# Kernel tuning notes

Hardware: AMD Instinct MI355X
Metric: run time of the kernel (lower is better)

## Reference

```python
import jax, jax.numpy as jnp
import numpy as np


def setup_inputs() -> dict:
    key = jax.random.key(0)
    k1, k2, k3 = jax.random.split(key, 3)
    B, T, S, D = 16, 1024, 1024, 1024
    inp = jax.random.normal(k1, (B, T, D), dtype=jnp.float32)
    ctx = jax.random.normal(k2, (B, S, D), dtype=jnp.float32)
    # nn.Linear(dim, dim, bias=False) weight, applied as x @ W.T
    W_in = jax.random.normal(k3, (D, D), dtype=jnp.float32) * (1.0 / np.sqrt(D))
    return {"input": inp, "context": ctx, "W_in": W_in}


def reference(input, context, W_in):
    # h_t = linear_in(input): [B,T,D] @ W_in.T
    h_t = jnp.einsum("btd,ed->bte", input, W_in)
    # align scores: [B,T,S]
    align = jnp.einsum("btd,bsd->bts", h_t, context)
    align_vectors = jax.nn.softmax(align, axis=-1)
    # context-weighted sum: [B,T,D]
    attn_h = jnp.einsum("bts,bsd->btd", align_vectors, context)
    # non-one-step path: transpose(0,1)
    attn_h = jnp.transpose(attn_h, (1, 0, 2))          # [T,B,D]
    align_vectors = jnp.transpose(align_vectors, (1, 0, 2))  # [T,B,S]
    return attn_h, align_vectors
```

## Files before the change

kernel.cpp:

```cpp
#include <hip/hip_runtime.h>
#include <hip/hip_bf16.h>

using short8 = __attribute__((ext_vector_type(8))) short;
using half8  = __attribute__((ext_vector_type(8))) _Float16;
using f32x4  = __attribute__((ext_vector_type(4))) float;

constexpr int Bdim = 16;
constexpr int Tdim = 1024;
constexpr int Sdim = 1024;
constexpr int Ddim = 1024;

__device__ __forceinline__ unsigned short f2hu(float x) {
  _Float16 h = (_Float16)x;
  return __builtin_bit_cast(unsigned short, h);
}
__device__ __forceinline__ float hu2f(unsigned short u) {
  return (float)__builtin_bit_cast(_Float16, u);
}

__global__ void __launch_bounds__(256)
conv_kernel(const float* __restrict__ src, unsigned short* __restrict__ dst, int n4) {
  int i = blockIdx.x * blockDim.x + threadIdx.x;
  int stride = gridDim.x * blockDim.x;
  for (; i < n4; i += stride) {
    float4 v = reinterpret_cast<const float4*>(src)[i];
    ushort4 h;
    h.x = f2hu(v.x); h.y = f2hu(v.y); h.z = f2hu(v.z); h.w = f2hu(v.w);
    reinterpret_cast<ushort4*>(dst)[i] = h;
  }
}

__global__ void __launch_bounds__(256)
ctxprep_kernel(const float* __restrict__ ctx, unsigned short* __restrict__ ctx16,
               unsigned short* __restrict__ ctxT) {
  __shared__ float tile[64][65];
  int b = blockIdx.z;
  int d0 = blockIdx.x * 64, s0 = blockIdx.y * 64;
  const float* src = ctx + (size_t)b * Sdim * Ddim;
  unsigned short* dstS = ctx16 + (size_t)b * Sdim * Ddim;
  unsigned short* dstT = ctxT + (size_t)b * Ddim * Sdim;
  int tx = threadIdx.x & 15, ty = threadIdx.x >> 4;
  #pragma unroll
  for (int r = 0; r < 4; ++r) {
    int s = ty + r * 16;
    float4 v = reinterpret_cast<const float4*>(src + (size_t)(s0 + s) * Ddim + d0)[tx];
    ushort4 hs;
    hs.x = f2hu(v.x); hs.y = f2hu(v.y); hs.z = f2hu(v.z); hs.w = f2hu(v.w);
    reinterpret_cast<ushort4*>(dstS + (size_t)(s0 + s) * Ddim + d0)[tx] = hs;
    tile[s][tx * 4 + 0] = v.x; tile[s][tx * 4 + 1] = v.y;
    tile[s][tx * 4 + 2] = v.z; tile[s][tx * 4 + 3] = v.w;
  }
  __syncthreads();
  #pragma unroll
  for (int r = 0; r < 4; ++r) {
    int d = ty + r * 16;
    ushort4 o;
    o.x = f2hu(tile[tx * 4 + 0][d]);
    o.y = f2hu(tile[tx * 4 + 1][d]);
    o.z = f2hu(tile[tx * 4 + 2][d]);
    o.w = f2hu(tile[tx * 4 + 3][d]);
    reinterpret_cast<ushort4*>(dstT + (size_t)(d0 + d) * Sdim + s0)[tx] = o;
  }
}

__device__ __forceinline__ short8 fragr(const unsigned short* t, int row, int g0) {
  int pg = g0 ^ ((row >> 1) & 3);
  return *reinterpret_cast<const short8*>(t + row * 32 + pg * 8);
}

#define MFMAH(d, x, y)                                                          \
  d = __builtin_amdgcn_mfma_f32_16x16x32_f16(__builtin_bit_cast(half8, (x)),    \
                                             __builtin_bit_cast(half8, (y)), (d), 0, 0, 0)

#define GLOADLDS(g, l)                                                          \
  __builtin_amdgcn_global_load_lds((const __attribute__((address_space(1))) void*)(g), \
                                   (__attribute__((address_space(3))) void*)(l), 16, 0, 0)

template <int MODE>
__global__ void __launch_bounds__(512, 2)
gemmP(const unsigned short* __restrict__ Ag, const unsigned short* __restrict__ Bg,
      size_t aBatch, size_t bBatch, int mnShift,
      unsigned short* __restrict__ outHi, unsigned short* __restrict__ outLo,
      float* __restrict__ outF) {
  constexpr int NT = 16;
  __shared__ __align__(16) unsigned short lds[2 * 2 * 16384];

  const int hw = blockIdx.x;
  const int L  = (hw & 7) * 32 + (hw >> 3);
  const int bb = L >> mnShift;
  const int r  = L & ((1 << mnShift) - 1);
  const int m0 = (r >> 2) * 256;
  const int n0 = (r & 3) * 256;

  const int tid  = threadIdx.x;
  const int lane = tid & 63;
  const int w    = tid >> 6;
  const int wr   = (w >> 2) * 128;
  const int wc   = (w & 3) * 64;
  const int l15  = lane & 15;
  const int g0   = lane >> 4;
  const int r7   = l15 & 7;

  const int srow8 = tid >> 3;
  const int sg    = tid & 7;
  const int rs    = srow8 & 7;
  const unsigned short* spA = Ag + (size_t)bb * aBatch + (size_t)(m0 + srow8) * 1024 + ((sg ^ rs) * 8);
  const unsigned short* spB = Bg + (size_t)bb * bBatch + (size_t)(n0 + srow8) * 1024 + ((sg ^ rs) * 8);

  auto stage = [&](int buf, int kt) {
    #pragma unroll
    for (int i = 0; i < 4; ++i) {
      unsigned short* lb = lds + buf * 32768 + (srow8 + i * 64) * 64 + sg * 8;
      GLOADLDS(spA + (size_t)i * (64 * 1024) + kt * 64, lb);
      GLOADLDS(spB + (size_t)i * (64 * 1024) + kt * 64, lb + 16384);
    }
  };

  f32x4 acc[8][4];
  const f32x4 vzero = {0.f, 0.f, 0.f, 0.f};
  #pragma unroll
  for (int f = 0; f < 8; ++f)
    #pragma unroll
    for (int j = 0; j < 4; ++j) acc[f][j] = vzero;

  stage(0, 0);

  #pragma unroll 1
  for (int t = 0; t < NT; ++t) {
    stage((t + 1) & 1, (t + 1 < NT) ? (t + 1) : (NT - 1));
    asm volatile("s_waitcnt vmcnt(8)" ::: "memory");
    __builtin_amdgcn_s_barrier();
    asm volatile("" ::: "memory");
    const unsigned short* tb = lds + (t & 1) * 32768;
    const unsigned short* tB = tb + 16384;

    short8 bf[4][2];
    #pragma unroll
    for (int j = 0; j < 4; ++j)
      #pragma unroll
      for (int kk = 0; kk < 2; ++kk) {
        const int row = wc + j * 16 + l15;
        bf[j][kk] = *reinterpret_cast<const short8*>(tB + row * 64 + ((kk * 4 + g0) ^ r7) * 8);
      }
    #pragma unroll
    for (int fp = 0; fp < 4; ++fp) {
      short8 af[2][2];
      #pragma unroll
      for (int f2 = 0; f2 < 2; ++f2) {
        const int row = wr + (fp * 2 + f2) * 16 + l15;
        #pragma unroll
        for (int kk = 0; kk < 2; ++kk)
          af[f2][kk] = *reinterpret_cast<const short8*>(tb + row * 64 + ((kk * 4 + g0) ^ r7) * 8);
      }
      __builtin_amdgcn_s_setprio(1);
      #pragma unroll
      for (int f2 = 0; f2 < 2; ++f2)
        #pragma unroll
        for (int j = 0; j < 4; ++j)
          #pragma unroll
          for (int kk = 0; kk < 2; ++kk)
            MFMAH(acc[fp * 2 + f2][j], af[f2][kk], bf[j][kk]);
      __builtin_amdgcn_s_setprio(0);
    }
    asm volatile("s_waitcnt lgkmcnt(0)" ::: "memory");
    __builtin_amdgcn_sched_barrier(0);
    __builtin_amdgcn_s_barrier();
  }

  const int lr = (lane >> 4) * 4;
  const int lc = lane & 15;
  #pragma unroll
  for (int f = 0; f < 8; ++f)
    #pragma unroll
    for (int j = 0; j < 4; ++j)
      #pragma unroll
      for (int q = 0; q < 4; ++q) {
        int rr = m0 + wr + f * 16 + lr + q;
        int cc = n0 + wc + j * 16 + lc;
        float v = acc[f][j][q];
        if constexpr (MODE == 0) {
          unsigned short h = f2hu(v);
          unsigned short l = f2hu(v - hu2f(h));
          outHi[(size_t)rr * 1024 + cc] = h;
          outLo[(size_t)rr * 1024 + cc] = l;
        } else {
          outF[((size_t)rr * 16 + bb) * 1024 + cc] = v;
        }
      }
}

__global__ void __launch_bounds__(512, 2)
gemmU(const unsigned short* __restrict__ Ah, const unsigned short* __restrict__ Al,
      const unsigned short* __restrict__ Bh,
      size_t aBatch, size_t bBatch, int mnShift,
      float* __restrict__ outF) {
  constexpr int OPS = 3;
  constexpr int BUFSTRIDE = OPS * 8192;
  constexpr int NT = 32;
  __shared__ __align__(16) unsigned short lds[3 * BUFSTRIDE];

  const int hw = blockIdx.x;
  const int L  = (hw & 7) * 32 + (hw >> 3);
  const int bb = L >> mnShift;
  const int r  = L & ((1 << mnShift) - 1);
  const int m0 = (r >> 2) * 256;
  const int n0 = (r & 3) * 256;

  const int tid  = threadIdx.x;
  const int lane = tid & 63;
  const int w    = tid >> 6;
  const int wr   = (w >> 2) * 128;
  const int wc   = (w & 3) * 64;
  const int l15  = lane & 15;
  const int g0   = lane >> 4;

  const int srow = tid >> 2;
  const int scol = ((tid & 3) ^ ((srow >> 1) & 3)) * 8;
  const unsigned short* sp[3];
  {
    const size_t aOff = (size_t)bb * aBatch + (size_t)(m0 + srow) * 1024 + scol;
    const size_t bOff = (size_t)bb * bBatch + (size_t)(n0 + srow) * 1024 + scol;
    sp[0] = Ah + aOff; sp[1] = Al + aOff; sp[2] = Bh + bOff;
  }

  auto stage_tile = [&](int buf, int kt) {
    #pragma unroll
    for (int op = 0; op < OPS; ++op)
      #pragma unroll
      for (int h = 0; h < 2; ++h) {
        const unsigned short* g = sp[op] + (size_t)h * (128 * 1024) + kt * 32;
        unsigned short* l = lds + buf * BUFSTRIDE + op * 8192 + h * 4096 + tid * 8;
        GLOADLDS(g, l);
      }
  };

  f32x4 acc[8][4];
  const f32x4 vzero = {0.f, 0.f, 0.f, 0.f};
  #pragma unroll
  for (int f = 0; f < 8; ++f)
    #pragma unroll
    for (int j = 0; j < 4; ++j) acc[f][j] = vzero;

  short8 ah[4], al[4], b0[2], b1[2];

  stage_tile(0, 0);
  stage_tile(1, 1);

  #pragma unroll 1
  for (int t = 0; t < NT; ++t) {
    const unsigned short* tb = lds + (t % 3) * BUFSTRIDE;
    const unsigned short* tA = tb;
    const unsigned short* tAl = tb + 8192;
    const unsigned short* tB = tb + 16384;

    stage_tile((t + 2) % 3, (t + 2 < NT) ? (t + 2) : (NT - 1));
    asm volatile("s_waitcnt vmcnt(12)" ::: "memory");
    __builtin_amdgcn_s_barrier();
    asm volatile("" ::: "memory");

    #pragma unroll
    for (int f = 0; f < 4; ++f) {
      ah[f] = fragr(tA, wr + f * 16 + l15, g0);
      al[f] = fragr(tAl, wr + f * 16 + l15, g0);
    }
    #pragma unroll
    for (int j = 0; j < 2; ++j) b0[j] = fragr(tB, wc + j * 16 + l15, g0);
    __builtin_amdgcn_s_setprio(1);
    #pragma unroll
    for (int f = 0; f < 4; ++f)
      #pragma unroll
      for (int j = 0; j < 2; ++j) { MFMAH(acc[f][j], ah[f], b0[j]); MFMAH(acc[f][j], al[f], b0[j]); }
    __builtin_amdgcn_s_setprio(0);

    #pragma unroll
    for (int j = 0; j < 2; ++j) b1[j] = fragr(tB, wc + (j + 2) * 16 + l15, g0);
    __builtin_amdgcn_s_setprio(1);
    #pragma unroll
    for (int f = 0; f < 4; ++f)
      #pragma unroll
      for (int j = 0; j < 2; ++j) { MFMAH(acc[f][j + 2], ah[f], b1[j]); MFMAH(acc[f][j + 2], al[f], b1[j]); }
    __builtin_amdgcn_s_setprio(0);

    #pragma unroll
    for (int f = 0; f < 4; ++f) {
      ah[f] = fragr(tA, wr + 64 + f * 16 + l15, g0);
      al[f] = fragr(tAl, wr + 64 + f * 16 + l15, g0);
    }
    __builtin_amdgcn_s_setprio(1);
    #pragma unroll
    for (int f = 0; f < 4; ++f)
      #pragma unroll
      for (int j = 0; j < 2; ++j) { MFMAH(acc[4 + f][j], ah[f], b0[j]); MFMAH(acc[4 + f][j], al[f], b0[j]); }
    __builtin_amdgcn_s_setprio(0);

    __builtin_amdgcn_s_setprio(1);
    #pragma unroll
    for (int f = 0; f < 4; ++f)
      #pragma unroll
      for (int j = 0; j < 2; ++j) { MFMAH(acc[4 + f][j + 2], ah[f], b1[j]); MFMAH(acc[4 + f][j + 2], al[f], b1[j]); }
    __builtin_amdgcn_s_setprio(0);
    asm volatile("" ::: "memory");
    __builtin_amdgcn_s_barrier();
  }

  const int lr = (lane >> 4) * 4;
  const int lc = lane & 15;
  #pragma unroll
  for (int f = 0; f < 8; ++f)
    #pragma unroll
    for (int j = 0; j < 4; ++j)
      #pragma unroll
      for (int q = 0; q < 4; ++q) {
        int rr = m0 + wr + f * 16 + lr + q;
        int cc = n0 + wc + j * 16 + lc;
        outF[((size_t)rr * 16 + bb) * 1024 + cc] = acc[f][j][q];
      }
}

__global__ void __launch_bounds__(256)
softmax_kernel(float* __restrict__ av, unsigned short* __restrict__ p) {
  int row = blockIdx.x;
  int t = row >> 4, b = row & 15;
  float* a = av + (size_t)row * 1024;
  int tid = threadIdx.x, lane = tid & 63, wid = tid >> 6;
  float4 v = reinterpret_cast<float4*>(a)[tid];
  float mx = fmaxf(fmaxf(v.x, v.y), fmaxf(v.z, v.w));
  #pragma unroll
  for (int o = 1; o < 64; o <<= 1) mx = fmaxf(mx, __shfl_xor(mx, o));
  __shared__ float redM[4], redS[4];
  if (lane == 0) redM[wid] = mx;
  __syncthreads();
  mx = fmaxf(fmaxf(redM[0], redM[1]), fmaxf(redM[2], redM[3]));
  float e0 = __expf(v.x - mx), e1 = __expf(v.y - mx);
  float e2 = __expf(v.z - mx), e3 = __expf(v.w - mx);
  float s = (e0 + e1) + (e2 + e3);
  #pragma unroll
  for (int o = 1; o < 64; o <<= 1) s += __shfl_xor(s, o);
  if (lane == 0) redS[wid] = s;
  __syncthreads();
  s = (redS[0] + redS[1]) + (redS[2] + redS[3]);
  float inv = 1.0f / s;
  float4 o4;
  o4.x = e0 * inv; o4.y = e1 * inv; o4.z = e2 * inv; o4.w = e3 * inv;
  reinterpret_cast<float4*>(a)[tid] = o4;
  ushort4 pb;
  pb.x = f2hu(o4.x); pb.y = f2hu(o4.y); pb.z = f2hu(o4.z); pb.w = f2hu(o4.w);
  reinterpret_cast<ushort4*>(p + ((size_t)b * Tdim + t) * Sdim)[tid] = pb;
}

extern "C" void kernel_launch(void* const* d_in, const int* in_sizes, int n_in,
                              void* d_out, int out_size, void* d_ws, size_t ws_size,
                              hipStream_t stream) {
  const float* input = (const float*)d_in[0];
  const float* ctx   = (const float*)d_in[1];
  const float* Wt    = (const float*)d_in[2];
  float* attn_out  = (float*)d_out;
  float* align_out = attn_out + (size_t)Tdim * Bdim * Ddim;

  const size_t NE = (size_t)Bdim * Tdim * Ddim;
  unsigned short* x16 = (unsigned short*)d_ws;
  unsigned short* Wh  = x16 + NE;
  unsigned short* hh  = Wh + (size_t)Ddim * Ddim;
  unsigned short* hl  = hh + NE;
  unsigned short* ctxT = hl + NE;
  unsigned short* ctx16 = x16;
  unsigned short* p     = hh;

  conv_kernel<<<2048, 256, 0, stream>>>(input, x16, (int)(NE / 4));
  conv_kernel<<<512, 256, 0, stream>>>(Wt, Wh, (int)((size_t)Ddim * Ddim / 4));
  gemmP<0><<<256, 512, 0, stream>>>(x16, Wh, 0, 0, 8, hh, hl, nullptr);
  ctxprep_kernel<<<dim3(16, 16, Bdim), 256, 0, stream>>>(ctx, ctx16, ctxT);
  gemmU<<<256, 512, 0, stream>>>(hh, hl, ctx16, (size_t)Tdim * Ddim,
                                 (size_t)Sdim * Ddim, 4, align_out);
  softmax_kernel<<<Bdim * Tdim, 256, 0, stream>>>(align_out, p);
  gemmP<1><<<256, 512, 0, stream>>>(p, ctxT, (size_t)Tdim * Sdim,
                                    (size_t)Ddim * Sdim, 4, nullptr, nullptr, attn_out);
}
```

Baseline: 220.5 us.

## Restructure align GEMM with K=64 tiles, double-buffered A and single-buffered B

Replaces the triple-buffered K=32 align-score GEMM with a K=64 version. The hi/lo A tiles are double-buffered, while the B (context) tile sits in a single buffer that is refilled mid-iteration once every wave holds its B fragments in registers. This halves the number of main-loop iterations and barriers and uses a wider XOR swizzle for the 64-wide rows. In exchange it adds an extra barrier per iteration, keeps more fragments live in registers, and exposes the B load latency inside the loop.

```diff
diff --git a/kernel.cpp b/kernel.cpp
--- a/kernel.cpp
+++ b/kernel.cpp
@@ -61,11 +61,6 @@
     o.w = f2hu(tile[tx * 4 + 3][d]);
     reinterpret_cast<ushort4*>(dstT + (size_t)(d0 + d) * Sdim + s0)[tx] = o;
   }
-}
-
-__device__ __forceinline__ short8 fragr(const unsigned short* t, int row, int g0) {
-  int pg = g0 ^ ((row >> 1) & 3);
-  return *reinterpret_cast<const short8*>(t + row * 32 + pg * 8);
 }
 
 #define MFMAH(d, x, y)                                                          \
@@ -190,14 +185,12 @@
 }
 
 __global__ void __launch_bounds__(512, 2)
-gemmU(const unsigned short* __restrict__ Ah, const unsigned short* __restrict__ Al,
+gemmS(const unsigned short* __restrict__ Ah, const unsigned short* __restrict__ Al,
       const unsigned short* __restrict__ Bh,
       size_t aBatch, size_t bBatch, int mnShift,
       float* __restrict__ outF) {
-  constexpr int OPS = 3;
-  constexpr int BUFSTRIDE = OPS * 8192;
-  constexpr int NT = 32;
-  __shared__ __align__(16) unsigned short lds[3 * BUFSTRIDE];
+  constexpr int NT = 16;
+  __shared__ __align__(16) unsigned short lds[5 * 16384];
 
   const int hw = blockIdx.x;
   const int L  = (hw & 7) * 32 + (hw >> 3);
@@ -213,25 +206,30 @@
   const int wc   = (w & 3) * 64;
   const int l15  = lane & 15;
   const int g0   = lane >> 4;
-
-  const int srow = tid >> 2;
-  const int scol = ((tid & 3) ^ ((srow >> 1) & 3)) * 8;
-  const unsigned short* sp[3];
-  {
-    const size_t aOff = (size_t)bb * aBatch + (size_t)(m0 + srow) * 1024 + scol;
-    const size_t bOff = (size_t)bb * bBatch + (size_t)(n0 + srow) * 1024 + scol;
-    sp[0] = Ah + aOff; sp[1] = Al + aOff; sp[2] = Bh + bOff;
-  }
-
-  auto stage_tile = [&](int buf, int kt) {
-    #pragma unroll
-    for (int op = 0; op < OPS; ++op)
-      #pragma unroll
-      for (int h = 0; h < 2; ++h) {
-        const unsigned short* g = sp[op] + (size_t)h * (128 * 1024) + kt * 32;
-        unsigned short* l = lds + buf * BUFSTRIDE + op * 8192 + h * 4096 + tid * 8;
-        GLOADLDS(g, l);
-      }
+  const int r7   = l15 & 7;
+
+  const int srow8 = tid >> 3;
+  const int sg    = tid & 7;
+  const int rs    = srow8 & 7;
+  const size_t aRow = (size_t)bb * aBatch + (size_t)(m0 + srow8) * 1024 + ((sg ^ rs) * 8);
+  const unsigned short* spAh = Ah + aRow;
+  const unsigned short* spAl = Al + aRow;
+  const unsigned short* spB  = Bh + (size_t)bb * bBatch + (size_t)(n0 + srow8) * 1024 + ((sg ^ rs) * 8);
+
+  auto stageA = [&](int buf, int kt) {
+    #pragma unroll
+    for (int i = 0; i < 4; ++i) {
+      unsigned short* lb = lds + buf * 32768 + (srow8 + i * 64) * 64 + sg * 8;
+      GLOADLDS(spAh + (size_t)i * (64 * 1024) + kt * 64, lb);
+      GLOADLDS(spAl + (size_t)i * (64 * 1024) + kt * 64, lb + 16384);
+    }
+  };
+  auto stageB = [&](int kt) {
+    #pragma unroll
+    for (int i = 0; i < 4; ++i) {
+      unsigned short* lb = lds + 65536 + (srow8 + i * 64) * 64 + sg * 8;
+      GLOADLDS(spB + (size_t)i * (64 * 1024) + kt * 64, lb);
+    }
   };
 
   f32x4 acc[8][4];
@@ -241,65 +239,82 @@
     #pragma unroll
     for (int j = 0; j < 4; ++j) acc[f][j] = vzero;
 
-  short8 ah[4], al[4], b0[2], b1[2];
-
-  stage_tile(0, 0);
-  stage_tile(1, 1);
+  stageA(0, 0);
+  stageB(0);
 
   #pragma unroll 1
   for (int t = 0; t < NT; ++t) {
-    const unsigned short* tb = lds + (t % 3) * BUFSTRIDE;
-    const unsigned short* tA = tb;
-    const unsigned short* tAl = tb + 8192;
-    const unsigned short* tB = tb + 16384;
-
-    stage_tile((t + 2) % 3, (t + 2 < NT) ? (t + 2) : (NT - 1));
-    asm volatile("s_waitcnt vmcnt(12)" ::: "memory");
+    const int tn = (t + 1 < NT) ? t + 1 : NT - 1;
+    stageA((t + 1) & 1, tn);
+    asm volatile("s_waitcnt vmcnt(8)" ::: "memory");
     __builtin_amdgcn_s_barrier();
     asm volatile("" ::: "memory");
-
-    #pragma unroll
-    for (int f = 0; f < 4; ++f) {
-      ah[f] = fragr(tA, wr + f * 16 + l15, g0);
-      al[f] = fragr(tAl, wr + f * 16 + l15, g0);
-    }
-    #pragma unroll
-    for (int j = 0; j < 2; ++j) b0[j] = fragr(tB, wc + j * 16 + l15, g0);
+    const unsigned short* tA  = lds + (t & 1) * 32768;
+    const unsigned short* tAl = tA + 16384;
+    const unsigned short* tB  = lds + 65536;
+
+    short8 bf[4][2];
+    #pragma unroll
+    for (int j = 0; j < 4; ++j)
+      #pragma unroll
+      for (int kk = 0; kk < 2; ++kk) {
+        const int row = wc + j * 16 + l15;
+        bf[j][kk] = *reinterpret_cast<const short8*>(tB + row * 64 + ((kk * 4 + g0) ^ r7) * 8);
+      }
+    short8 ah0[2][2], al0[2][2];
+    #pragma unroll
+    for (int f2 = 0; f2 < 2; ++f2) {
+      const int row = wr + f2 * 16 + l15;
+      #pragma unroll
+      for (int kk = 0; kk < 2; ++kk) {
+        const int po = ((kk * 4 + g0) ^ r7) * 8;
+        ah0[f2][kk] = *reinterpret_cast<const short8*>(tA  + row * 64 + po);
+        al0[f2][kk] = *reinterpret_cast<const short8*>(tAl + row * 64 + po);
+      }
+    }
+    asm volatile("s_waitcnt lgkmcnt(0)" ::: "memory");
+    __builtin_amdgcn_sched_barrier(0);
+    __builtin_amdgcn_s_barrier();
+    stageB(tn);
     __builtin_amdgcn_s_setprio(1);
     #pragma unroll
-    for (int f = 0; f < 4; ++f)
-      #pragma unroll
-      for (int j = 0; j < 2; ++j) { MFMAH(acc[f][j], ah[f], b0[j]); MFMAH(acc[f][j], al[f], b0[j]); }
+    for (int f2 = 0; f2 < 2; ++f2)
+      #pragma unroll
+      for (int j = 0; j < 4; ++j)
+        #pragma unroll
+        for (int kk = 0; kk < 2; ++kk) {
+          MFMAH(acc[f2][j], ah0[f2][kk], bf[j][kk]);
+          MFMAH(acc[f2][j], al0[f2][kk], bf[j][kk]);
+        }
     __builtin_amdgcn_s_setprio(0);
 
     #pragma unroll
-    for (int j = 0; j < 2; ++j) b1[j] = fragr(tB, wc + (j + 2) * 16 + l15, g0);
-    __builtin_amdgcn_s_setprio(1);
-    #pragma unroll
-    for (int f = 0; f < 4; ++f)
-      #pragma unroll
-      for (int j = 0; j < 2; ++j) { MFMAH(acc[f][j + 2], ah[f], b1[j]); MFMAH(acc[f][j + 2], al[f], b1[j]); }
-    __builtin_amdgcn_s_setprio(0);
-
-    #pragma unroll
-    for (int f = 0; f < 4; ++f) {
-      ah[f] = fragr(tA, wr + 64 + f * 16 + l15, g0);
-      al[f] = fragr(tAl, wr + 64 + f * 16 + l15, g0);
-    }
-    __builtin_amdgcn_s_setprio(1);
-    #pragma unroll
-    for (int f = 0; f < 4; ++f)
-      #pragma unroll
-      for (int j = 0; j < 2; ++j) { MFMAH(acc[4 + f][j], ah[f], b0[j]); MFMAH(acc[4 + f][j], al[f], b0[j]); }
-    __builtin_amdgcn_s_setprio(0);
-
-    __builtin_amdgcn_s_setprio(1);
-    #pragma unroll
-    for (int f = 0; f < 4; ++f)
-      #pragma unroll
-      for (int j = 0; j < 2; ++j) { MFMAH(acc[4 + f][j + 2], ah[f], b1[j]); MFMAH(acc[4 + f][j + 2], al[f], b1[j]); }
-    __builtin_amdgcn_s_setprio(0);
-    asm volatile("" ::: "memory");
+    for (int fp = 1; fp < 4; ++fp) {
+      short8 ah[2][2], al[2][2];
+      #pragma unroll
+      for (int f2 = 0; f2 < 2; ++f2) {
+        const int row = wr + (fp * 2 + f2) * 16 + l15;
+        #pragma unroll
+        for (int kk = 0; kk < 2; ++kk) {
+          const int po = ((kk * 4 + g0) ^ r7) * 8;
+          ah[f2][kk] = *reinterpret_cast<const short8*>(tA  + row * 64 + po);
+          al[f2][kk] = *reinterpret_cast<const short8*>(tAl + row * 64 + po);
+        }
+      }
+      __builtin_amdgcn_s_setprio(1);
+      #pragma unroll
+      for (int f2 = 0; f2 < 2; ++f2)
+        #pragma unroll
+        for (int j = 0; j < 4; ++j)
+          #pragma unroll
+          for (int kk = 0; kk < 2; ++kk) {
+            MFMAH(acc[fp * 2 + f2][j], ah[f2][kk], bf[j][kk]);
+            MFMAH(acc[fp * 2 + f2][j], al[f2][kk], bf[j][kk]);
+          }
+      __builtin_amdgcn_s_setprio(0);
+    }
+    asm volatile("s_waitcnt lgkmcnt(0)" ::: "memory");
+    __builtin_amdgcn_sched_barrier(0);
     __builtin_amdgcn_s_barrier();
   }
 
@@ -370,7 +385,7 @@
   conv_kernel<<<512, 256, 0, stream>>>(Wt, Wh, (int)((size_t)Ddim * Ddim / 4));
   gemmP<0><<<256, 512, 0, stream>>>(x16, Wh, 0, 0, 8, hh, hl, nullptr);
   ctxprep_kernel<<<dim3(16, 16, Bdim), 256, 0, stream>>>(ctx, ctx16, ctxT);
-  gemmU<<<256, 512, 0, stream>>>(hh, hl, ctx16, (size_t)Tdim * Ddim,
+  gemmS<<<256, 512, 0, stream>>>(hh, hl, ctx16, (size_t)Tdim * Ddim,
                                  (size_t)Sdim * Ddim, 4, align_out);
   softmax_kernel<<<Bdim * Tdim, 256, 0, stream>>>(align_out, p);
   gemmP<1><<<256, 512, 0, stream>>>(p, ctxT, (size_t)Tdim * Sdim,
```

Result: no change. 218.4 us (-1.0%).
